# Kernel optimization log

Hardware: AMD Instinct MI355X
Metric: run time of the kernel (lower is better)

The kernel has to match this reference:

```python
import jax, jax.numpy as jnp
import numpy as np

def setup_inputs() -> dict:
    key = jax.random.key(0)
    k1, k2, k3, k4 = jax.random.split(key, 4)
    B, T, C, D = 4, 4096, 1024, 128
    x = jax.random.normal(k1, (B, T, C), dtype=jnp.float32)
    Wq = jax.random.normal(k2, (C, D), dtype=jnp.float32) * (C ** -0.5)
    Wk = jax.random.normal(k3, (C, D), dtype=jnp.float32) * (C ** -0.5)
    Wv = jax.random.normal(k4, (C, D), dtype=jnp.float32) * (C ** -0.5)
    return {"x": x, "Wq": Wq, "Wk": Wk, "Wv": Wv}

def reference(x, Wq, Wk, Wv):
    # x: [B,T,C]; Wq/Wk/Wv: [C,D] (nn.Linear bias=False => x @ W)
    B, T, C = x.shape
    q = jnp.einsum('btc,cd->btd', x, Wq)  # [B,T,D]
    k = jnp.einsum('btc,cd->btd', x, Wk)
    v = jnp.einsum('btc,cd->btd', x, Wv)
    dk = q.shape[-1]
    scale = dk ** -0.5
    w = jnp.einsum('btd,bsd->bts', q, k) * scale  # [B,T,T]
    causal = jnp.tril(jnp.ones((T, T), dtype=bool))
    w = jnp.where(causal, w, -jnp.inf)
    w = jax.nn.softmax(w, axis=-1)
    # dropout p=0.0 => identity
    attention = jnp.einsum('bts,bsd->btd', w, v)  # [B,T,D]
    return attention
```

## Files before the change

### kernel.cpp

```cpp
#include <hip/hip_runtime.h>
#include <stdint.h>

typedef __bf16 bf16_t;
typedef bf16_t bf16x8 __attribute__((ext_vector_type(8)));
typedef float f32x4 __attribute__((ext_vector_type(4)));
typedef unsigned short us8 __attribute__((ext_vector_type(8)));
typedef unsigned short us4 __attribute__((ext_vector_type(4)));
typedef unsigned int u32x4 __attribute__((ext_vector_type(4)));

#define B_ 4
#define T_ 4096
#define C_ 1024
#define D_ 128

#define NCHUNK_PB 288
#define QSCALE 0.12751744f
#define M0 14.0f

__device__ __forceinline__ uint16_t f2bf(float f) {
    union { float f; uint32_t u; } v; v.f = f;
    uint32_t u = v.u;
    uint32_t r = (u + 0x7fffu + ((u >> 16) & 1u)) >> 16;
    return (uint16_t)r;
}

__device__ __forceinline__ uint16_t bfru(float f) {
    return (uint16_t)((__float_as_uint(f) + 0x8000u) >> 16);
}

__device__ __forceinline__ float bf2f(uint16_t u) {
    return __uint_as_float((uint32_t)u << 16);
}

__global__ __launch_bounds__(256) void prep_w(const float* __restrict__ Wq,
                                              const float* __restrict__ Wk,
                                              const float* __restrict__ Wv,
                                              uint16_t* __restrict__ WT) {
    int idx = blockIdx.x * 256 + threadIdx.x;
    if (idx >= 3 * D_ * C_) return;
    int w   = idx / (D_ * C_);
    int rem = idx - w * (D_ * C_);
    int n   = rem / C_;
    int k   = rem - n * C_;
    const float* W = (w == 0) ? Wq : (w == 1) ? Wk : Wv;
    WT[idx] = f2bf(W[(size_t)k * D_ + n]);
}

#define GST 72

__global__ __launch_bounds__(256) void qkv_gemm(const float* __restrict__ x,
                                                const uint16_t* __restrict__ WT,
                                                uint16_t* __restrict__ qb,
                                                uint16_t* __restrict__ kb,
                                                uint16_t* __restrict__ vT) {
    __shared__ __align__(16) uint16_t A_lds[64 * GST];
    __shared__ __align__(16) uint16_t W_lds[128 * GST];

    int tid  = threadIdx.x;
    int lane = tid & 63;
    int wave = tid >> 6;
    int quad = lane >> 4;
    int lx   = lane & 15;
    int wm   = wave >> 1, wn = wave & 1;

    int bx   = blockIdx.x;
    int wsel = bx % 3;
    int m0   = (bx / 3) * 64;
    const uint16_t* Wp = WT + (size_t)wsel * (D_ * C_);

    f32x4 acc[2][4];
    for (int mf = 0; mf < 2; mf++)
        for (int nf = 0; nf < 4; nf++)
            acc[mf][nf] = (f32x4){0.f, 0.f, 0.f, 0.f};

    int arow = tid >> 2, acb = (tid & 3) * 16;
    int wrow = tid >> 1, wcb = (tid & 1) * 32;

    for (int k0 = 0; k0 < C_; k0 += 64) {
        {
            const float* xp = x + (size_t)(m0 + arow) * C_ + k0 + acb;
            uint32_t d[8];
#pragma unroll
            for (int j = 0; j < 4; j++) {
                float4 f = *(const float4*)(xp + j * 4);
                uint32_t u0 = __float_as_uint(f.x) + 0x8000u;
                uint32_t u1 = __float_as_uint(f.y) + 0x8000u;
                uint32_t u2 = __float_as_uint(f.z) + 0x8000u;
                uint32_t u3 = __float_as_uint(f.w) + 0x8000u;
                d[2 * j]     = __builtin_amdgcn_perm(u1, u0, 0x07060302);
                d[2 * j + 1] = __builtin_amdgcn_perm(u3, u2, 0x07060302);
            }
            *(u32x4*)&A_lds[arow * GST + acb]     = (u32x4){d[0], d[1], d[2], d[3]};
            *(u32x4*)&A_lds[arow * GST + acb + 8] = (u32x4){d[4], d[5], d[6], d[7]};
        }
        {
            const uint16_t* wp = Wp + (size_t)wrow * C_ + k0 + wcb;
#pragma unroll
            for (int i = 0; i < 4; i++)
                *(us8*)&W_lds[wrow * GST + wcb + i * 8] = *(const us8*)(wp + i * 8);
        }
        __syncthreads();

#pragma unroll
        for (int kc = 0; kc < 2; kc++) {
            bf16x8 af[2];
#pragma unroll
            for (int mf = 0; mf < 2; mf++)
                af[mf] = *(const bf16x8*)&A_lds[(wm * 32 + mf * 16 + lx) * GST + kc * 32 + quad * 8];
#pragma unroll
            for (int nf = 0; nf < 4; nf++) {
                bf16x8 bf = *(const bf16x8*)&W_lds[(wn * 64 + nf * 16 + lx) * GST + kc * 32 + quad * 8];
                acc[0][nf] = __builtin_amdgcn_mfma_f32_16x16x32_bf16(af[0], bf, acc[0][nf], 0, 0, 0);
                acc[1][nf] = __builtin_amdgcn_mfma_f32_16x16x32_bf16(af[1], bf, acc[1][nf], 0, 0, 0);
            }
        }
        __syncthreads();
    }

    int mrow0 = m0 + wm * 32 + quad * 4;
    if (wsel == 2) {
#pragma unroll
        for (int mf = 0; mf < 2; mf++) {
            int mbase = mrow0 + mf * 16;
            int batch = mbase >> 12;
            int t     = mbase & 4095;
#pragma unroll
            for (int nf = 0; nf < 4; nf++) {
                int n = wn * 64 + nf * 16 + lx;
                us4 pv;
#pragma unroll
                for (int r = 0; r < 4; r++) pv[r] = bfru(acc[mf][nf][r]);
                *(us4*)&vT[(size_t)batch * D_ * T_ + (size_t)n * T_ + t] = pv;
            }
        }
    } else {
        uint16_t* dst = (wsel == 0) ? qb : kb;
        float sc = (wsel == 0) ? QSCALE : 1.0f;
#pragma unroll
        for (int mf = 0; mf < 2; mf++)
#pragma unroll
            for (int nf = 0; nf < 4; nf++) {
                int n = wn * 64 + nf * 16 + lx;
#pragma unroll
                for (int r = 0; r < 4; r++)
                    dst[(size_t)(mrow0 + mf * 16 + r) * D_ + n] = bfru(acc[mf][nf][r] * sc);
            }
    }
}

__global__ __launch_bounds__(256, 4) void attn(const uint16_t* __restrict__ qb,
                                               const uint16_t* __restrict__ kb,
                                               const uint16_t* __restrict__ vT,
                                               uint16_t* __restrict__ part,
                                               float* __restrict__ ml) {
    __shared__ __align__(16) uint16_t K_lds[64 * 128];
    __shared__ __align__(16) uint16_t V_lds[128 * 64];
    __shared__ __align__(16) uint16_t P_lds[4 * 16 * 64];

    int tid  = threadIdx.x;
    int lane = tid & 63;
    int wave = tid >> 6;
    int quad = lane >> 4;
    int lx   = lane & 15;
    int lx7  = lx & 7;

    int batch = blockIdx.x & 3;
    int L     = NCHUNK_PB - 1 - (blockIdx.x >> 2);
    int g = 0;
    while (g < 7 && 4 * (g + 1) * (g + 2) <= L) g++;
    int rem   = L - 4 * g * (g + 1);
    int jt    = 8 * g + rem / (g + 1);
    int chunk = rem - (rem / (g + 1)) * (g + 1);
    int lidx  = batch * NCHUNK_PB + L;

    int q0     = jt * 64;
    int st0    = chunk * 8;
    int ntiles = min(8, jt - st0 + 1);

    bf16x8 qf[4];
    {
        const uint16_t* qp = qb + (size_t)(batch * T_ + q0 + wave * 16 + lx) * D_ + quad * 8;
#pragma unroll
        for (int kc = 0; kc < 4; kc++) qf[kc] = *(const bf16x8*)(qp + kc * 32);
    }

    f32x4 o[8];
    for (int i = 0; i < 8; i++) o[i] = (f32x4){0.f, 0.f, 0.f, 0.f};
    float l_i[4] = {0.f, 0.f, 0.f, 0.f};

    int krow = tid >> 2, kc0 = (tid & 3) * 4;
    int vd   = tid >> 1, vc0 = (tid & 1) * 4;

    for (int it = 0; it < ntiles; it++) {
        int s0 = (st0 + it) * 64;
        {
            const uint16_t* kp = kb + (size_t)(batch * T_ + s0 + krow) * D_ + kc0 * 8;
#pragma unroll
            for (int i = 0; i < 4; i++)
                *(us8*)&K_lds[krow * 128 + (((kc0 + i) ^ (krow & 7)) * 8)] = *(const us8*)(kp + i * 8);
        }
        {
            const uint16_t* vp = vT + (size_t)batch * D_ * T_ + (size_t)vd * T_ + s0 + vc0 * 8;
#pragma unroll
            for (int i = 0; i < 4; i++)
                *(us8*)&V_lds[vd * 64 + (((vc0 + i) ^ (vd & 7)) * 8)] = *(const us8*)(vp + i * 8);
        }
        __syncthreads();

        f32x4 s[4];
        for (int nf = 0; nf < 4; nf++) s[nf] = (f32x4){0.f, 0.f, 0.f, 0.f};
#pragma unroll
        for (int kc = 0; kc < 4; kc++)
#pragma unroll
            for (int nf = 0; nf < 4; nf++) {
                bf16x8 kf = *(const bf16x8*)&K_lds[(nf * 16 + lx) * 128 + (((kc * 4 + quad) ^ lx7) * 8)];
                s[nf] = __builtin_amdgcn_mfma_f32_16x16x32_bf16(qf[kc], kf, s[nf], 0, 0, 0);
            }

        float p[4][4];
#pragma unroll
        for (int nf = 0; nf < 4; nf++)
#pragma unroll
            for (int r = 0; r < 4; r++) p[nf][r] = s[nf][r];

        if (st0 + it == jt) {
            int rowg = q0 + wave * 16 + quad * 4;
#pragma unroll
            for (int nf = 0; nf < 4; nf++) {
                int colg = s0 + nf * 16 + lx;
#pragma unroll
                for (int r = 0; r < 4; r++)
                    if (colg > rowg + r) p[nf][r] = -INFINITY;
            }
        }

#pragma unroll
        for (int nf = 0; nf < 4; nf++)
#pragma unroll
            for (int r = 0; r < 4; r++)
                p[nf][r] = exp2f(p[nf][r] - M0);
#pragma unroll
        for (int r = 0; r < 4; r++)
            l_i[r] += (p[0][r] + p[1][r]) + (p[2][r] + p[3][r]);

#pragma unroll
        for (int nf = 0; nf < 4; nf++)
#pragma unroll
            for (int r = 0; r < 4; r++) {
                uint32_t u  = __float_as_uint(p[nf][r]) + 0x8000u;
                uint32_t pu = (uint32_t)__shfl_xor((int)u, 1, 64);
                uint32_t pk = __builtin_amdgcn_perm(pu, u, 0x07060302);
                if ((lane & 1) == 0) {
                    int prow = quad * 4 + r;
                    int pchk = nf * 2 + (lx >> 3);
                    *(uint32_t*)&P_lds[wave * 1024 + prow * 64 + ((pchk ^ (prow & 7)) * 8) + lx7] = pk;
                }
            }

        bf16x8 pf[2];
        pf[0] = *(const bf16x8*)&P_lds[wave * 1024 + lx * 64 + ((quad ^ lx7) * 8)];
        pf[1] = *(const bf16x8*)&P_lds[wave * 1024 + lx * 64 + (((4 + quad) ^ lx7) * 8)];
#pragma unroll
        for (int nf = 0; nf < 8; nf++)
#pragma unroll
            for (int kc = 0; kc < 2; kc++) {
                bf16x8 vf = *(const bf16x8*)&V_lds[(nf * 16 + lx) * 64 + (((kc * 4 + quad) ^ lx7) * 8)];
                o[nf] = __builtin_amdgcn_mfma_f32_16x16x32_bf16(pf[kc], vf, o[nf], 0, 0, 0);
            }
        __syncthreads();
    }

#pragma unroll
    for (int off = 1; off < 16; off <<= 1)
#pragma unroll
        for (int r = 0; r < 4; r++)
            l_i[r] += __shfl_xor(l_i[r], off, 64);

    uint16_t* pp = part + (size_t)lidx * (64 * 128);
#pragma unroll
    for (int nf = 0; nf < 8; nf++)
#pragma unroll
        for (int r = 0; r < 4; r++) {
            int lrow = wave * 16 + quad * 4 + r;
            pp[lrow * 128 + nf * 16 + lx] = bfru(o[nf][r]);
        }
    if (lx == 0) {
#pragma unroll
        for (int r = 0; r < 4; r++)
            ml[(size_t)lidx * 64 + wave * 16 + quad * 4 + r] = l_i[r];
    }
}

__global__ __launch_bounds__(256) void combine(const uint16_t* __restrict__ part,
                                               const float* __restrict__ ml,
                                               float* __restrict__ out) {
    int bidx  = blockIdx.x;
    int batch = bidx >> 6;
    int jt    = bidx & 63;
    int g     = jt >> 3;
    int base  = batch * NCHUNK_PB + jt + g * (jt - 4 * g - 4);
    int nch   = g + 1;

    int tid  = threadIdx.x;
    int lrow = tid >> 2;
    int c0   = (tid & 3) * 32;

    float Lsum = 0.f;
    f32x4 acc[8];
#pragma unroll
    for (int i = 0; i < 8; i++) acc[i] = (f32x4){0.f, 0.f, 0.f, 0.f};

    for (int c = 0; c < nch; c++) {
        Lsum += ml[(size_t)(base + c) * 64 + lrow];
        const uint16_t* p = part + (size_t)(base + c) * (64 * 128) + lrow * 128 + c0;
#pragma unroll
        for (int i = 0; i < 4; i++) {
            us8 v = *(const us8*)(p + i * 8);
#pragma unroll
            for (int j = 0; j < 8; j++)
                acc[i * 2 + (j >> 2)][j & 3] += bf2f(v[j]);
        }
    }
    float inv = 1.f / Lsum;
    size_t row = (size_t)(batch * T_ + jt * 64 + lrow);
#pragma unroll
    for (int i = 0; i < 8; i++)
        *(f32x4*)(out + row * 128 + c0 + i * 4) = acc[i] * inv;
}

extern "C" void kernel_launch(void* const* d_in, const int* in_sizes, int n_in,
                              void* d_out, int out_size, void* d_ws, size_t ws_size,
                              hipStream_t stream) {
    const float* x  = (const float*)d_in[0];
    const float* Wq = (const float*)d_in[1];
    const float* Wk = (const float*)d_in[2];
    const float* Wv = (const float*)d_in[3];
    float* out = (float*)d_out;

    uint16_t* ws = (uint16_t*)d_ws;
    uint16_t* qb = ws;
    uint16_t* kb = qb + (size_t)16384 * 128;
    uint16_t* vT = kb + (size_t)16384 * 128;
    uint16_t* WT = vT + (size_t)16384 * 128;
    uint16_t* part = WT + (size_t)3 * D_ * C_;
    float* ml = (float*)(part + (size_t)4 * NCHUNK_PB * 64 * 128);

    prep_w<<<dim3((3 * D_ * C_ + 255) / 256), dim3(256), 0, stream>>>(Wq, Wk, Wv, WT);
    qkv_gemm<<<dim3(3 * (16384 / 64)), dim3(256), 0, stream>>>(x, WT, qb, kb, vT);
    attn<<<dim3(B_ * NCHUNK_PB), dim3(256), 0, stream>>>(qb, kb, vT, part, ml);
    combine<<<dim3(B_ * (T_ / 64)), dim3(256), 0, stream>>>(part, ml, out);
}
```

Measured before the change: 205.6 us.

## Register-prefetch next K/V tile, raise MFMA wave priority, split combine columns

In the attention kernel, the next K and V tiles are loaded from global memory into registers while the current tile is being computed, so global load latency overlaps the MFMA work. MFMA sections are wrapped in s_setprio to favour waves that are issuing matrix ops. The combine kernel is split into two blocks per query tile, each handling half the columns, which doubles its block count and halves per-thread work. The prefetch costs extra VGPRs (8 x us8) and may reduce occupancy.

```diff
diff --git a/kernel.cpp b/kernel.cpp
--- a/kernel.cpp
+++ b/kernel.cpp
@@ -191,24 +191,40 @@
     int krow = tid >> 2, kc0 = (tid & 3) * 4;
     int vd   = tid >> 1, vc0 = (tid & 1) * 4;
 
+    const uint16_t* kbase = kb + (size_t)(batch * T_ + krow) * D_ + kc0 * 8;
+    const uint16_t* vbase = vT + (size_t)batch * D_ * T_ + (size_t)vd * T_ + vc0 * 8;
+
+    us8 kreg[4], vreg[4];
+    {
+        const uint16_t* kp = kbase + (size_t)(st0 * 64) * D_;
+        const uint16_t* vp = vbase + st0 * 64;
+#pragma unroll
+        for (int i = 0; i < 4; i++) kreg[i] = *(const us8*)(kp + i * 8);
+#pragma unroll
+        for (int i = 0; i < 4; i++) vreg[i] = *(const us8*)(vp + i * 8);
+    }
+
     for (int it = 0; it < ntiles; it++) {
         int s0 = (st0 + it) * 64;
-        {
-            const uint16_t* kp = kb + (size_t)(batch * T_ + s0 + krow) * D_ + kc0 * 8;
-#pragma unroll
-            for (int i = 0; i < 4; i++)
-                *(us8*)&K_lds[krow * 128 + (((kc0 + i) ^ (krow & 7)) * 8)] = *(const us8*)(kp + i * 8);
-        }
-        {
-            const uint16_t* vp = vT + (size_t)batch * D_ * T_ + (size_t)vd * T_ + s0 + vc0 * 8;
-#pragma unroll
-            for (int i = 0; i < 4; i++)
-                *(us8*)&V_lds[vd * 64 + (((vc0 + i) ^ (vd & 7)) * 8)] = *(const us8*)(vp + i * 8);
+#pragma unroll
+        for (int i = 0; i < 4; i++)
+            *(us8*)&K_lds[krow * 128 + (((kc0 + i) ^ (krow & 7)) * 8)] = kreg[i];
+#pragma unroll
+        for (int i = 0; i < 4; i++)
+            *(us8*)&V_lds[vd * 64 + (((vc0 + i) ^ (vd & 7)) * 8)] = vreg[i];
+        if (it + 1 < ntiles) {
+            const uint16_t* kp = kbase + (size_t)(s0 + 64) * D_;
+            const uint16_t* vp = vbase + (s0 + 64);
+#pragma unroll
+            for (int i = 0; i < 4; i++) kreg[i] = *(const us8*)(kp + i * 8);
+#pragma unroll
+            for (int i = 0; i < 4; i++) vreg[i] = *(const us8*)(vp + i * 8);
         }
         __syncthreads();
 
         f32x4 s[4];
         for (int nf = 0; nf < 4; nf++) s[nf] = (f32x4){0.f, 0.f, 0.f, 0.f};
+        __builtin_amdgcn_s_setprio(1);
 #pragma unroll
         for (int kc = 0; kc < 4; kc++)
 #pragma unroll
@@ -216,6 +232,7 @@
                 bf16x8 kf = *(const bf16x8*)&K_lds[(nf * 16 + lx) * 128 + (((kc * 4 + quad) ^ lx7) * 8)];
                 s[nf] = __builtin_amdgcn_mfma_f32_16x16x32_bf16(qf[kc], kf, s[nf], 0, 0, 0);
             }
+        __builtin_amdgcn_s_setprio(0);
 
         float p[4][4];
 #pragma unroll
@@ -260,6 +277,7 @@
         bf16x8 pf[2];
         pf[0] = *(const bf16x8*)&P_lds[wave * 1024 + lx * 64 + ((quad ^ lx7) * 8)];
         pf[1] = *(const bf16x8*)&P_lds[wave * 1024 + lx * 64 + (((4 + quad) ^ lx7) * 8)];
+        __builtin_amdgcn_s_setprio(1);
 #pragma unroll
         for (int nf = 0; nf < 8; nf++)
 #pragma unroll
@@ -267,6 +285,7 @@
                 bf16x8 vf = *(const bf16x8*)&V_lds[(nf * 16 + lx) * 64 + (((kc * 4 + quad) ^ lx7) * 8)];
                 o[nf] = __builtin_amdgcn_mfma_f32_16x16x32_bf16(pf[kc], vf, o[nf], 0, 0, 0);
             }
+        __builtin_amdgcn_s_setprio(0);
         __syncthreads();
     }
 
@@ -295,26 +314,27 @@
                                                const float* __restrict__ ml,
                                                float* __restrict__ out) {
     int bidx  = blockIdx.x;
-    int batch = bidx >> 6;
-    int jt    = bidx & 63;
+    int half  = bidx & 1;
+    int jt    = (bidx >> 1) & 63;
+    int batch = bidx >> 7;
     int g     = jt >> 3;
     int base  = batch * NCHUNK_PB + jt + g * (jt - 4 * g - 4);
     int nch   = g + 1;
 
     int tid  = threadIdx.x;
     int lrow = tid >> 2;
-    int c0   = (tid & 3) * 32;
+    int c0   = half * 64 + (tid & 3) * 16;
 
     float Lsum = 0.f;
-    f32x4 acc[8];
-#pragma unroll
-    for (int i = 0; i < 8; i++) acc[i] = (f32x4){0.f, 0.f, 0.f, 0.f};
+    f32x4 acc[4];
+#pragma unroll
+    for (int i = 0; i < 4; i++) acc[i] = (f32x4){0.f, 0.f, 0.f, 0.f};
 
     for (int c = 0; c < nch; c++) {
         Lsum += ml[(size_t)(base + c) * 64 + lrow];
         const uint16_t* p = part + (size_t)(base + c) * (64 * 128) + lrow * 128 + c0;
 #pragma unroll
-        for (int i = 0; i < 4; i++) {
+        for (int i = 0; i < 2; i++) {
             us8 v = *(const us8*)(p + i * 8);
 #pragma unroll
             for (int j = 0; j < 8; j++)
@@ -324,7 +344,7 @@
     float inv = 1.f / Lsum;
     size_t row = (size_t)(batch * T_ + jt * 64 + lrow);
 #pragma unroll
-    for (int i = 0; i < 8; i++)
+    for (int i = 0; i < 4; i++)
         *(f32x4*)(out + row * 128 + c0 + i * 4) = acc[i] * inv;
 }
 
@@ -348,5 +368,5 @@
     prep_w<<<dim3((3 * D_ * C_ + 255) / 256), dim3(256), 0, stream>>>(Wq, Wk, Wv, WT);
     qkv_gemm<<<dim3(3 * (16384 / 64)), dim3(256), 0, stream>>>(x, WT, qb, kb, vT);
     attn<<<dim3(B_ * NCHUNK_PB), dim3(256), 0, stream>>>(qb, kb, vT, part, ml);
-    combine<<<dim3(B_ * (T_ / 64)), dim3(256), 0, stream>>>(part, ml, out);
-}
+    combine<<<dim3(B_ * (T_ / 64) * 2), dim3(256), 0, stream>>>(part, ml, out);
+}
```

Result: slower. 255.6 us (+24.3%).
